# Kernel tuning notes

Hardware: AMD Instinct MI355X
Metric: run time of the kernel (lower is better)

The kernel has to match this reference:

```python
import jax, jax.numpy as jnp
import numpy as np

B, S, D, H = 2, 2048, 1024, 16
DK = D // H


def setup_inputs() -> dict:
    key = jax.random.key(0)
    ks = jax.random.split(key, 11)
    scale = 1.0 / np.sqrt(D)
    inp = {
        "query": jax.random.normal(ks[0], (B, S, D), dtype=jnp.float32),
        "key": jax.random.normal(ks[1], (B, S, D), dtype=jnp.float32),
        "value": jax.random.normal(ks[2], (B, S, D), dtype=jnp.float32),
        "Wq": jax.random.normal(ks[3], (D, D), dtype=jnp.float32) * scale,
        "bq": jnp.zeros((D,), dtype=jnp.float32),
        "Wk": jax.random.normal(ks[4], (D, D), dtype=jnp.float32) * scale,
        "bk": jnp.zeros((D,), dtype=jnp.float32),
        "Wv": jax.random.normal(ks[5], (D, D), dtype=jnp.float32) * scale,
        "bv": jnp.zeros((D,), dtype=jnp.float32),
        "Wo": jax.random.normal(ks[6], (D, D), dtype=jnp.float32) * scale,
        "bo": jnp.zeros((D,), dtype=jnp.float32),
    }
    return inp


def _split_heads(x):
    # [B,S,D] -> [B,H,S,DK]
    b, s, _ = x.shape
    return x.reshape(b, s, H, DK).transpose(0, 2, 1, 3)


def reference(query, key, value, Wq, bq, Wk, bk, Wv, bv, Wo, bo):
    q = _split_heads(query @ Wq.T + bq)
    k = _split_heads(key @ Wk.T + bk)
    v = _split_heads(value @ Wv.T + bv)
    # scaled dot-product attention: [B,H,S,S]
    scores = jnp.einsum("bhqd,bhkd->bhqk", q, k) / np.sqrt(DK).astype(np.float32)
    attn = jax.nn.softmax(scores, axis=-1)  # stable max-subtract softmax, same math
    ctx = jnp.einsum("bhqk,bhkd->bhqd", attn, v)  # [B,H,S,DK]
    ctx = ctx.transpose(0, 2, 1, 3).reshape(query.shape[0], -1, H * DK)
    return ctx @ Wo.T + bo
```

## Files before the change

### kernel.cpp

```cpp
#include <hip/hip_runtime.h>
#include <math.h>

constexpr int NB = 2;
constexpr int NS = 2048;
constexpr int ND = 1024;
constexpr int NH = 16;
constexpr int NDK = 64;

typedef __attribute__((ext_vector_type(8))) short short8;
typedef __attribute__((ext_vector_type(4))) float floatx4;

__device__ inline unsigned short f2bf(float x) {
    unsigned u = __builtin_bit_cast(unsigned, x);
    u += 0x7fffu + ((u >> 16) & 1u);
    return (unsigned short)(u >> 16);
}

__device__ inline uint4 pack8(float4 a, float4 b) {
    unsigned short t[8] = {f2bf(a.x), f2bf(a.y), f2bf(a.z), f2bf(a.w),
                           f2bf(b.x), f2bf(b.y), f2bf(b.z), f2bf(b.w)};
    return *(uint4*)t;
}

#define GLOAD_LDS16(g, l) __builtin_amdgcn_global_load_lds( \
    (const __attribute__((address_space(1))) void*)(g),     \
    (__attribute__((address_space(3))) void*)(l), 16, 0, 0)

#define QSCALE 0.18033688f

__global__ __launch_bounds__(256) void cvt_all(
    const float* __restrict__ s0, const float* __restrict__ s1,
    const float* __restrict__ s2, const float* __restrict__ s3,
    const float* __restrict__ s4, const float* __restrict__ s5,
    const float* __restrict__ s6,
    unsigned short* __restrict__ d0, unsigned short* __restrict__ d1,
    unsigned short* __restrict__ d2, unsigned short* __restrict__ d3,
    unsigned short* __restrict__ d4, unsigned short* __restrict__ d5,
    unsigned short* __restrict__ d6)
{
    const int y = blockIdx.y;
    const float* srcs[7] = {s0, s1, s2, s3, s4, s5, s6};
    unsigned short* dsts[7] = {d0, d1, d2, d3, d4, d5, d6};
    const int nel = (y < 3) ? NB * NS * ND : ND * ND;
    int i = (blockIdx.x * 256 + threadIdx.x) * 8;
    if (i >= nel) return;
    const float* s = srcs[y];
    unsigned short* d = dsts[y];
    float4 a = *(const float4*)(s + i);
    float4 b = *(const float4*)(s + i + 4);
    *(uint4*)(d + i) = pack8(a, b);
}

template<int QA, int QB>
__device__ __forceinline__ void mfma_quad(
    floatx4 (&acc)[8][4], const short8 (&ta)[4][2], const short8 (&tb)[2][2][2])
{
#pragma unroll
    for (int ii = 0; ii < 4; ++ii)
#pragma unroll
        for (int jj = 0; jj < 2; ++jj) {
            acc[QA * 4 + ii][QB * 2 + jj] = __builtin_amdgcn_mfma_f32_16x16x32_bf16(
                ta[ii][0], tb[QB][jj][0], acc[QA * 4 + ii][QB * 2 + jj], 0, 0, 0);
            acc[QA * 4 + ii][QB * 2 + jj] = __builtin_amdgcn_mfma_f32_16x16x32_bf16(
                ta[ii][1], tb[QB][jj][1], acc[QA * 4 + ii][QB * 2 + jj], 0, 0, 0);
        }
}

__global__ __launch_bounds__(512, 2) void gemm_qkv(
    const unsigned short* __restrict__ Xq, const unsigned short* __restrict__ Xk,
    const unsigned short* __restrict__ Xv,
    const unsigned short* __restrict__ Wq, const unsigned short* __restrict__ Wk,
    const unsigned short* __restrict__ Wv,
    const float* __restrict__ bq, const float* __restrict__ bk,
    const float* __restrict__ bv,
    unsigned short* __restrict__ Cq, unsigned short* __restrict__ Ck,
    unsigned short* __restrict__ Cv)
{
    __shared__ unsigned short As[2][256 * 64];
    __shared__ unsigned short Bs[2][256 * 64];

    const int tid = threadIdx.x, w = tid >> 6, lane = tid & 63;
    const int lo = lane & 15, quad = lane >> 4;
    const int bid = blockIdx.x;
    const int seg = bid >> 6;
    const int idx = bid & 63;
    const int xcd = idx & 7;
    const int t8  = idx >> 3;
    const int K = ND;

    int bm, bn;
    const unsigned short *A, *Bw;
    const float* bias;
    if (seg == 2) {
        bm = t8 & 3; bn = (t8 >> 2) * 8 + xcd;
        A = Wv; Bw = Xv; bias = bv;
    } else {
        bn = t8 & 3; bm = (t8 >> 2) * 8 + xcd;
        if (seg == 1) { A = Xk; Bw = Wk; bias = bk; }
        else          { A = Xq; Bw = Wq; bias = bq; }
    }

    const int WM = (w >> 2) * 128, WN = (w & 3) * 64;

    const int srow = tid >> 3;
    const int sgo  = ((tid & 7) ^ (srow & 7)) * 8;
    const unsigned short* Asrc = A  + (size_t)(bm * 256 + srow) * K + sgo;
    const unsigned short* Bsrc = Bw + (size_t)(bn * 256 + srow) * K + sgo;

#define SA(bf_, t_, s_) GLOAD_LDS16(Asrc + (size_t)(s_) * 64 * K + (t_) * 64, \
                                    &As[bf_][(s_) * 4096 + tid * 8])
#define SB(bf_, t_, s_) GLOAD_LDS16(Bsrc + (size_t)(s_) * 64 * K + (t_) * 64, \
                                    &Bs[bf_][(s_) * 4096 + tid * 8])

    const int rp0 = ((quad) ^ (lo & 7)) * 8;
    const int rp1 = ((4 + quad) ^ (lo & 7)) * 8;

    short8 ta[4][2], tb[2][2][2];

#define RDA(bf_, qa_) { _Pragma("unroll") \
    for (int ii = 0; ii < 4; ++ii) { \
        const unsigned short* p_ = &As[bf_][(WM + (qa_) * 64 + ii * 16 + lo) * 64]; \
        ta[ii][0] = *(const short8*)(p_ + rp0); \
        ta[ii][1] = *(const short8*)(p_ + rp1); } }
#define RDB(bf_, qb_) { _Pragma("unroll") \
    for (int jj = 0; jj < 2; ++jj) { \
        const unsigned short* p_ = &Bs[bf_][(WN + (qb_) * 32 + jj * 16 + lo) * 64]; \
        tb[qb_][jj][0] = *(const short8*)(p_ + rp0); \
        tb[qb_][jj][1] = *(const short8*)(p_ + rp1); } }

#define PH_SYNC1 __builtin_amdgcn_s_barrier(); \
    asm volatile("s_waitcnt lgkmcnt(0)" ::: "memory"); \
    __builtin_amdgcn_sched_barrier(0); \
    __builtin_amdgcn_s_setprio(1);
#define PH_SYNC2 __builtin_amdgcn_s_setprio(0); \
    __builtin_amdgcn_sched_barrier(0); \
    __builtin_amdgcn_s_barrier();

    floatx4 acc[8][4];
#pragma unroll
    for (int i = 0; i < 8; ++i)
#pragma unroll
        for (int j = 0; j < 4; ++j) acc[i][j] = (floatx4){0.f, 0.f, 0.f, 0.f};

    SB(0, 0, 0); SB(0, 0, 1); SB(0, 0, 2); SB(0, 0, 3);
    SA(0, 0, 0); SA(0, 0, 1); SA(0, 0, 2); SA(0, 0, 3);
    SB(1, 1, 0); SB(1, 1, 1); SB(1, 1, 2); SB(1, 1, 3);
    asm volatile("s_waitcnt vmcnt(4)" ::: "memory");
    __builtin_amdgcn_s_barrier();

    constexpr int NIT = ND / 128;
#pragma unroll 1
    for (int it = 0; it < NIT; ++it) {
        const bool nl = (it < NIT - 1);
        const int t1 = 2 * it + 1, t2 = 2 * it + 2, t3 = 2 * it + 3;

        RDA(0, 0); RDB(0, 0);
        SA(1, t1, 0); SA(1, t1, 1);
        PH_SYNC1; mfma_quad<0, 0>(acc, ta, tb); PH_SYNC2;

        RDB(0, 1);
        SA(1, t1, 2); SA(1, t1, 3);
        PH_SYNC1; mfma_quad<0, 1>(acc, ta, tb); PH_SYNC2;

        RDA(0, 1);
        if (nl) { SB(0, t2, 0); SB(0, t2, 1); }
        PH_SYNC1; mfma_quad<1, 1>(acc, ta, tb); PH_SYNC2;

        if (nl) { SB(0, t2, 2); SB(0, t2, 3); }
        if (nl) asm volatile("s_waitcnt vmcnt(4)" ::: "memory");
        else    asm volatile("s_waitcnt vmcnt(0)" ::: "memory");
        PH_SYNC1; mfma_quad<1, 0>(acc, ta, tb); PH_SYNC2;

        RDA(1, 0); RDB(1, 0);
        if (nl) { SA(0, t2, 0); SA(0, t2, 1); }
        PH_SYNC1; mfma_quad<0, 0>(acc, ta, tb); PH_SYNC2;

        RDB(1, 1);
        if (nl) { SA(0, t2, 2); SA(0, t2, 3); }
        PH_SYNC1; mfma_quad<0, 1>(acc, ta, tb); PH_SYNC2;

        RDA(1, 1);
        if (nl) { SB(1, t3, 0); SB(1, t3, 1); }
        PH_SYNC1; mfma_quad<1, 1>(acc, ta, tb); PH_SYNC2;

        if (nl) { SB(1, t3, 2); SB(1, t3, 3); }
        if (nl) asm volatile("s_waitcnt vmcnt(4)" ::: "memory");
        PH_SYNC1; mfma_quad<1, 0>(acc, ta, tb); PH_SYNC2;
    }

#undef SA
#undef SB
#undef RDA
#undef RDB
#undef PH_SYNC1
#undef PH_SYNC2

    if (seg < 2) {
        unsigned short* C = seg ? Ck : Cq;
        const float scale = seg ? 1.f : QSCALE;
#pragma unroll
        for (int j = 0; j < 4; ++j) {
            const int col = bn * 256 + WN + j * 16 + lo;
            const float bb = bias[col];
#pragma unroll
            for (int i = 0; i < 8; ++i)
#pragma unroll
                for (int r = 0; r < 4; ++r) {
                    const int row = bm * 256 + WM + i * 16 + quad * 4 + r;
                    C[(size_t)row * ND + col] = f2bf((acc[i][j][r] + bb) * scale);
                }
        }
    } else {
#pragma unroll
        for (int i = 0; i < 8; ++i)
#pragma unroll
            for (int r = 0; r < 4; ++r) {
                const int row = bm * 256 + WM + i * 16 + quad * 4 + r;
                const float bb = bias[row];
#pragma unroll
                for (int j = 0; j < 4; ++j) {
                    const int col = bn * 256 + WN + j * 16 + lo;
                    const int b = col >> 11, s = col & (NS - 1);
                    Cv[(size_t)(b * ND + row) * NS + s] = f2bf(acc[i][j][r] + bb);
                }
            }
    }
}

constexpr int PRS = 72;

__global__ __launch_bounds__(512, 4) void attn_mfma(
    const unsigned short* __restrict__ qb,
    const unsigned short* __restrict__ kb,
    const unsigned short* __restrict__ vt,
    float* __restrict__ cacc0, float* __restrict__ cacc1,
    float* __restrict__ lbuf)
{
    __shared__ unsigned short Ks[2][64 * 64];
    __shared__ unsigned short Vs[2][64 * 64];
    __shared__ unsigned short Pt[8][32 * PRS];

    const int tid = threadIdx.x, w = tid >> 6, lane = tid & 63;
    const int lo = lane & 15, quad = lane >> 4;
    const int bid = blockIdx.x;
    const int xcd = bid & 7;
    const int tt  = bid >> 3;
    const int qgrp = tt & 7;
    const int bhk  = (tt >> 3) * 8 + xcd;
    const int bh = bhk >> 1, ksp = bhk & 1;
    const int b = bh >> 4, h = bh & 15;
    const int q0 = qgrp * 256 + w * 32;

    short8 qf[2][2];
    #pragma unroll
    for (int qt = 0; qt < 2; ++qt) {
        const unsigned short* qrow =
            qb + (size_t)(b * NS + q0 + qt * 16 + lo) * ND + h * NDK + quad * 8;
        qf[qt][0] = *(const short8*)(qrow);
        qf[qt][1] = *(const short8*)(qrow + 32);
    }

    const int r0 = tid >> 3, g0 = (tid & 7) ^ (r0 & 7);
    const unsigned short* Ksrc = kb + (size_t)(b * NS + r0) * ND + h * NDK + g0 * 8;
    const unsigned short* Vsrc = vt + (size_t)(bh * NDK + r0) * NS + g0 * 8;

#define STAGE(bf_, k_) { \
    GLOAD_LDS16(Ksrc + (size_t)(k_) * ND, &Ks[bf_][tid * 8]); \
    GLOAD_LDS16(Vsrc + (k_),              &Vs[bf_][tid * 8]); }

    floatx4 acc[2][4], lacc[2];
    #pragma unroll
    for (int qt = 0; qt < 2; ++qt) {
        lacc[qt] = (floatx4){0.f, 0.f, 0.f, 0.f};
        #pragma unroll
        for (int cb = 0; cb < 4; ++cb) acc[qt][cb] = (floatx4){0.f, 0.f, 0.f, 0.f};
    }

    const short8 ones = {0x3F80, 0x3F80, 0x3F80, 0x3F80,
                         0x3F80, 0x3F80, 0x3F80, 0x3F80};
    unsigned short* pw = &Pt[w][0];
    const int pos0 = (quad ^ (lo & 7)) * 8;
    const int pos1 = ((4 + quad) ^ (lo & 7)) * 8;

    const int kbase = ksp * 1024;
    STAGE(0, kbase);

    #pragma unroll 2
    for (int it = 0; it < 16; ++it) {
        const int bf = it & 1;
        if (it < 15) {
            STAGE(bf ^ 1, kbase + (it + 1) * 64);
            asm volatile("s_waitcnt vmcnt(2)" ::: "memory");
        } else {
            asm volatile("s_waitcnt vmcnt(0)" ::: "memory");
        }
        __builtin_amdgcn_s_barrier();
        __builtin_amdgcn_sched_barrier(0);

        const unsigned short* Kc = Ks[bf];
        const unsigned short* Vc = Vs[bf];

        floatx4 s[2][4];
        __builtin_amdgcn_s_setprio(1);
        #pragma unroll
        for (int t = 0; t < 4; ++t) {
            const int rw = (t * 16 + lo) * 64;
            const short8 kf0 = *(const short8*)(Kc + rw + pos0);
            const short8 kf1 = *(const short8*)(Kc + rw + pos1);
            #pragma unroll
            for (int qt = 0; qt < 2; ++qt) {
                s[qt][t] = __builtin_amdgcn_mfma_f32_16x16x32_bf16(
                    kf0, qf[qt][0], (floatx4){0.f, 0.f, 0.f, 0.f}, 0, 0, 0);
                s[qt][t] = __builtin_amdgcn_mfma_f32_16x16x32_bf16(
                    kf1, qf[qt][1], s[qt][t], 0, 0, 0);
            }
        }
        __builtin_amdgcn_s_setprio(0);

        #pragma unroll
        for (int qt = 0; qt < 2; ++qt)
            #pragma unroll
            for (int t = 0; t < 4; ++t) {
                unsigned u0 = __builtin_bit_cast(unsigned, __builtin_amdgcn_exp2f(s[qt][t][0]));
                unsigned u1 = __builtin_bit_cast(unsigned, __builtin_amdgcn_exp2f(s[qt][t][1]));
                unsigned u2 = __builtin_bit_cast(unsigned, __builtin_amdgcn_exp2f(s[qt][t][2]));
                unsigned u3 = __builtin_bit_cast(unsigned, __builtin_amdgcn_exp2f(s[qt][t][3]));
                uint2 pk = {(u0 >> 16) | (u1 & 0xFFFF0000u),
                            (u2 >> 16) | (u3 & 0xFFFF0000u)};
                *(uint2*)(pw + (qt * 16 + lo) * PRS + t * 16 + quad * 4) = pk;
            }

        short8 pf[2][2];
        #pragma unroll
        for (int qt = 0; qt < 2; ++qt) {
            pf[qt][0] = *(const short8*)(pw + (qt * 16 + lo) * PRS + quad * 8);
            pf[qt][1] = *(const short8*)(pw + (qt * 16 + lo) * PRS + 32 + quad * 8);
            lacc[qt] = __builtin_amdgcn_mfma_f32_16x16x32_bf16(pf[qt][0], ones, lacc[qt], 0, 0, 0);
            lacc[qt] = __builtin_amdgcn_mfma_f32_16x16x32_bf16(pf[qt][1], ones, lacc[qt], 0, 0, 0);
        }

        __builtin_amdgcn_s_setprio(1);
        #pragma unroll
        for (int cb = 0; cb < 4; ++cb) {
            const int rw = (cb * 16 + lo) * 64;
            const short8 vf0 = *(const short8*)(Vc + rw + pos0);
            const short8 vf1 = *(const short8*)(Vc + rw + pos1);
            #pragma unroll
            for (int qt = 0; qt < 2; ++qt) {
                acc[qt][cb] = __builtin_amdgcn_mfma_f32_16x16x32_bf16(pf[qt][0], vf0, acc[qt][cb], 0, 0, 0);
                acc[qt][cb] = __builtin_amdgcn_mfma_f32_16x16x32_bf16(pf[qt][1], vf1, acc[qt][cb], 0, 0, 0);
            }
        }
        __builtin_amdgcn_s_setprio(0);

        __builtin_amdgcn_sched_barrier(0);
        __builtin_amdgcn_s_barrier();
    }
#undef STAGE

    float* ca = ksp ? cacc1 : cacc0;
    float* lb = lbuf + (size_t)ksp * (NB * NH * NS);
    #pragma unroll
    for (int qt = 0; qt < 2; ++qt) {
        #pragma unroll
        for (int cb = 0; cb < 4; ++cb)
            #pragma unroll
            for (int r = 0; r < 4; ++r) {
                size_t off = (size_t)(b * NS + q0 + qt * 16 + quad * 4 + r) * ND
                           + h * NDK + cb * 16 + lo;
                ca[off] = acc[qt][cb][r];
            }
        if (lo == 0)
            #pragma unroll
            for (int r = 0; r < 4; ++r)
                lb[(size_t)bh * NS + q0 + qt * 16 + quad * 4 + r] = lacc[qt][r];
    }
}

__global__ __launch_bounds__(256) void gemm_o(
    const float* __restrict__ cacc0, const float* __restrict__ cacc1,
    const float* __restrict__ lbuf, const unsigned short* __restrict__ Bw,
    const float* __restrict__ bias, float* __restrict__ Cout)
{
    __shared__ unsigned short As[64 * 64];
    __shared__ unsigned short Bs[128 * 64];
    const int tid = threadIdx.x, w = tid >> 6, lane = tid & 63;
    const int lo = lane & 15, quad = lane >> 4;
    const int bid = blockIdx.x;
    const int xcd = bid & 7;
    const int tt  = bid >> 3;
    const int bn  = tt & 7;
    const int bm  = (tt >> 3) * 8 + xcd;
    const int K = ND;
    const int wm = (w >> 1) * 32, wn = (w & 1) * 64;
    const size_t LHALF = (size_t)NB * NH * NS;

    const int ar = tid >> 3;
    const int ag = (tid & 7) ^ (ar & 7);
    const int tok0 = bm * 64 + ar, tok1 = tok0 + 32;
    const float* A00 = cacc0 + (size_t)tok0 * ND + ag * 8;
    const float* A01 = cacc1 + (size_t)tok0 * ND + ag * 8;
    const float* A10 = cacc0 + (size_t)tok1 * ND + ag * 8;
    const float* A11 = cacc1 + (size_t)tok1 * ND + ag * 8;
    const size_t lb0 = (size_t)((tok0 >> 11) << 4) * NS + (tok0 & (NS - 1));
    const size_t lb1 = (size_t)((tok1 >> 11) << 4) * NS + (tok1 & (NS - 1));
    unsigned short* AsD0 = As + tid * 8;
    unsigned short* AsD1 = As + (tid + 256) * 8;

    const unsigned short* Bg[4];
    unsigned short* BsD[4];
    #pragma unroll
    for (int p = 0; p < 4; ++p) {
        int c = tid + 256 * p, r = c >> 3, g = (c & 7) ^ (r & 7);
        Bg[p] = Bw + (size_t)(bn * 128 + r) * K + g * 8;
        BsD[p] = Bs + c * 8;
    }

    floatx4 acc[2][4];
    #pragma unroll
    for (int i = 0; i < 2; ++i)
        #pragma unroll
        for (int j = 0; j < 4; ++j) acc[i][j] = (floatx4){0.f, 0.f, 0.f, 0.f};

    float4 ra[8];
    float lv0, lv1;
    ra[0] = *(const float4*)(A00);     ra[1] = *(const float4*)(A00 + 4);
    ra[2] = *(const float4*)(A01);     ra[3] = *(const float4*)(A01 + 4);
    ra[4] = *(const float4*)(A10);     ra[5] = *(const float4*)(A10 + 4);
    ra[6] = *(const float4*)(A11);     ra[7] = *(const float4*)(A11 + 4);
    lv0 = lbuf[lb0] + lbuf[lb0 + LHALF];
    lv1 = lbuf[lb1] + lbuf[lb1 + LHALF];

    for (int k0 = 0; k0 < K; k0 += 64) {
        const float inv0 = __builtin_amdgcn_rcpf(lv0);
        const float inv1 = __builtin_amdgcn_rcpf(lv1);
        __syncthreads();
        #pragma unroll
        for (int p = 0; p < 4; ++p) GLOAD_LDS16(Bg[p] + k0, BsD[p]);
        {
            float4 s0 = {(ra[0].x + ra[2].x) * inv0, (ra[0].y + ra[2].y) * inv0,
                         (ra[0].z + ra[2].z) * inv0, (ra[0].w + ra[2].w) * inv0};
            float4 s1 = {(ra[1].x + ra[3].x) * inv0, (ra[1].y + ra[3].y) * inv0,
                         (ra[1].z + ra[3].z) * inv0, (ra[1].w + ra[3].w) * inv0};
            *(uint4*)AsD0 = pack8(s0, s1);
            float4 s2 = {(ra[4].x + ra[6].x) * inv1, (ra[4].y + ra[6].y) * inv1,
                         (ra[4].z + ra[6].z) * inv1, (ra[4].w + ra[6].w) * inv1};
            float4 s3 = {(ra[5].x + ra[7].x) * inv1, (ra[5].y + ra[7].y) * inv1,
                         (ra[5].z + ra[7].z) * inv1, (ra[5].w + ra[7].w) * inv1};
            *(uint4*)AsD1 = pack8(s2, s3);
        }
        __syncthreads();

        const int kn = k0 + 64;
        if (kn < K) {
            ra[0] = *(const float4*)(A00 + kn); ra[1] = *(const float4*)(A00 + kn + 4);
            ra[2] = *(const float4*)(A01 + kn); ra[3] = *(const float4*)(A01 + kn + 4);
            ra[4] = *(const float4*)(A10 + kn); ra[5] = *(const float4*)(A10 + kn + 4);
            ra[6] = *(const float4*)(A11 + kn); ra[7] = *(const float4*)(A11 + kn + 4);
            const size_t hoff = (size_t)(kn >> 6) * NS;
            lv0 = lbuf[lb0 + hoff] + lbuf[lb0 + hoff + LHALF];
            lv1 = lbuf[lb1 + hoff] + lbuf[lb1 + hoff + LHALF];
        }

        #pragma unroll
        for (int s = 0; s < 2; ++s) {
            const int pos = ((s * 4 + quad) ^ (lo & 7)) * 8;
            short8 af[2], bf[4];
            #pragma unroll
            for (int i = 0; i < 2; ++i)
                af[i] = *(const short8*)(As + (wm + i * 16 + lo) * 64 + pos);
            #pragma unroll
            for (int j = 0; j < 4; ++j)
                bf[j] = *(const short8*)(Bs + (wn + j * 16 + lo) * 64 + pos);
            #pragma unroll
            for (int i = 0; i < 2; ++i)
                #pragma unroll
                for (int j = 0; j < 4; ++j)
                    acc[i][j] = __builtin_amdgcn_mfma_f32_16x16x32_bf16(af[i], bf[j], acc[i][j], 0, 0, 0);
        }
    }

    #pragma unroll
    for (int j = 0; j < 4; ++j) {
        const int col = bn * 128 + wn + j * 16 + lo;
        const float bb = bias[col];
        #pragma unroll
        for (int i = 0; i < 2; ++i)
            #pragma unroll
            for (int r = 0; r < 4; ++r) {
                const int row = bm * 64 + wm + i * 16 + quad * 4 + r;
                Cout[(size_t)row * ND + col] = acc[i][j][r] + bb;
            }
    }
}

extern "C" void kernel_launch(void* const* d_in, const int* in_sizes, int n_in,
                              void* d_out, int out_size, void* d_ws, size_t ws_size,
                              hipStream_t stream)
{
    const float* query = (const float*)d_in[0];
    const float* key   = (const float*)d_in[1];
    const float* value = (const float*)d_in[2];
    const float* Wq    = (const float*)d_in[3];
    const float* bq    = (const float*)d_in[4];
    const float* Wk    = (const float*)d_in[5];
    const float* bk    = (const float*)d_in[6];
    const float* Wv    = (const float*)d_in[7];
    const float* bv    = (const float*)d_in[8];
    const float* Wo    = (const float*)d_in[9];
    const float* bo    = (const float*)d_in[10];
    float* out = (float*)d_out;

    const size_t n  = (size_t)NB * NS * ND;
    const size_t nw = (size_t)ND * ND;

    unsigned short* X0   = (unsigned short*)d_ws;
    unsigned short* X1   = X0 + n;
    unsigned short* X2   = X1 + n;
    unsigned short* W0   = X2 + n;
    unsigned short* W1   = W0 + nw;
    unsigned short* W2   = W1 + nw;
    unsigned short* W3   = W2 + nw;
    unsigned short* qbuf = W3 + nw;
    unsigned short* kbuf = qbuf + n;
    unsigned short* vtb  = kbuf + n;
    float* cacc1 = (float*)(vtb + n);
    float* lbuf  = cacc1 + n;
    float* cacc0 = (float*)X1;

    cvt_all<<<dim3((int)(n / 2048), 7), 256, 0, stream>>>(
        query, key, value, Wq, Wk, Wv, Wo, X0, X1, X2, W0, W1, W2, W3);

    gemm_qkv<<<192, 512, 0, stream>>>(X0, X1, X2, W0, W1, W2,
                                      bq, bk, bv, qbuf, kbuf, vtb);

    attn_mfma<<<512, 512, 0, stream>>>(qbuf, kbuf, vtb, cacc0, cacc1, lbuf);

    gemm_o<<<512, 256, 0, stream>>>(cacc0, cacc1, lbuf, W3, bo, out);
}
```

Before: 220.0 us.

## Software-pipeline PV matmul one iteration behind exp to overlap MFMA with transcendental

Restructures the attention inner loop so that the P·V MFMAs (and the row-sum MFMAs) for the previous key block run interleaved with the exp2 computation of the current block. V gets a third LDS buffer, rotated by pointer each iteration, and the last block's PV is drained after the loop. The aim is to hide the serial exp/pack latency behind matrix-core work. The cost is extra LDS, live P fragments carried across iterations and more register pressure, which could hurt occupancy at 4 blocks per CU.

```diff
diff --git a/kernel.cpp b/kernel.cpp
--- a/kernel.cpp
+++ b/kernel.cpp
@@ -237,7 +237,7 @@
     float* __restrict__ lbuf)
 {
     __shared__ unsigned short Ks[2][64 * 64];
-    __shared__ unsigned short Vs[2][64 * 64];
+    __shared__ unsigned short Vs[3][64 * 64];
     __shared__ unsigned short Pt[8][32 * PRS];
 
     const int tid = threadIdx.x, w = tid >> 6, lane = tid & 63;
@@ -264,10 +264,6 @@
     const unsigned short* Ksrc = kb + (size_t)(b * NS + r0) * ND + h * NDK + g0 * 8;
     const unsigned short* Vsrc = vt + (size_t)(bh * NDK + r0) * NS + g0 * 8;
 
-#define STAGE(bf_, k_) { \
-    GLOAD_LDS16(Ksrc + (size_t)(k_) * ND, &Ks[bf_][tid * 8]); \
-    GLOAD_LDS16(Vsrc + (k_),              &Vs[bf_][tid * 8]); }
-
     floatx4 acc[2][4], lacc[2];
     #pragma unroll
     for (int qt = 0; qt < 2; ++qt) {
@@ -283,13 +279,20 @@
     const int pos1 = ((4 + quad) ^ (lo & 7)) * 8;
 
     const int kbase = ksp * 1024;
-    STAGE(0, kbase);
+    GLOAD_LDS16(Ksrc + (size_t)kbase * ND, &Ks[0][tid * 8]);
+    GLOAD_LDS16(Vsrc + kbase,              &Vs[0][tid * 8]);
+
+    unsigned short *vp = &Vs[2][0], *vc = &Vs[0][0], *vn = &Vs[1][0];
+
+    short8 pf[2][2];
 
     #pragma unroll 2
     for (int it = 0; it < 16; ++it) {
-        const int bf = it & 1;
+        const int kbuf = it & 1;
         if (it < 15) {
-            STAGE(bf ^ 1, kbase + (it + 1) * 64);
+            const int kk = kbase + (it + 1) * 64;
+            GLOAD_LDS16(Ksrc + (size_t)kk * ND, &Ks[kbuf ^ 1][tid * 8]);
+            GLOAD_LDS16(Vsrc + kk, &vn[tid * 8]);
             asm volatile("s_waitcnt vmcnt(2)" ::: "memory");
         } else {
             asm volatile("s_waitcnt vmcnt(0)" ::: "memory");
@@ -297,8 +300,7 @@
         __builtin_amdgcn_s_barrier();
         __builtin_amdgcn_sched_barrier(0);
 
-        const unsigned short* Kc = Ks[bf];
-        const unsigned short* Vc = Vs[bf];
+        const unsigned short* Kc = Ks[kbuf];
 
         floatx4 s[2][4];
         __builtin_amdgcn_s_setprio(1);
@@ -318,45 +320,62 @@
         __builtin_amdgcn_s_setprio(0);
 
         #pragma unroll
-        for (int qt = 0; qt < 2; ++qt)
-            #pragma unroll
-            for (int t = 0; t < 4; ++t) {
-                unsigned u0 = __builtin_bit_cast(unsigned, __builtin_amdgcn_exp2f(s[qt][t][0]));
-                unsigned u1 = __builtin_bit_cast(unsigned, __builtin_amdgcn_exp2f(s[qt][t][1]));
-                unsigned u2 = __builtin_bit_cast(unsigned, __builtin_amdgcn_exp2f(s[qt][t][2]));
-                unsigned u3 = __builtin_bit_cast(unsigned, __builtin_amdgcn_exp2f(s[qt][t][3]));
+        for (int cb = 0; cb < 4; ++cb) {
+            if (it > 0) {
+                const int rw = (cb * 16 + lo) * 64;
+                const short8 vf0 = *(const short8*)(vp + rw + pos0);
+                const short8 vf1 = *(const short8*)(vp + rw + pos1);
+                __builtin_amdgcn_s_setprio(1);
+                #pragma unroll
+                for (int qt = 0; qt < 2; ++qt) {
+                    acc[qt][cb] = __builtin_amdgcn_mfma_f32_16x16x32_bf16(
+                        pf[qt][0], vf0, acc[qt][cb], 0, 0, 0);
+                    acc[qt][cb] = __builtin_amdgcn_mfma_f32_16x16x32_bf16(
+                        pf[qt][1], vf1, acc[qt][cb], 0, 0, 0);
+                }
+                lacc[cb >> 1] = __builtin_amdgcn_mfma_f32_16x16x32_bf16(
+                    pf[cb >> 1][cb & 1], ones, lacc[cb >> 1], 0, 0, 0);
+                __builtin_amdgcn_s_setprio(0);
+            }
+            #pragma unroll
+            for (int qt = 0; qt < 2; ++qt) {
+                unsigned u0 = __builtin_bit_cast(unsigned, __builtin_amdgcn_exp2f(s[qt][cb][0]));
+                unsigned u1 = __builtin_bit_cast(unsigned, __builtin_amdgcn_exp2f(s[qt][cb][1]));
+                unsigned u2 = __builtin_bit_cast(unsigned, __builtin_amdgcn_exp2f(s[qt][cb][2]));
+                unsigned u3 = __builtin_bit_cast(unsigned, __builtin_amdgcn_exp2f(s[qt][cb][3]));
                 uint2 pk = {(u0 >> 16) | (u1 & 0xFFFF0000u),
                             (u2 >> 16) | (u3 & 0xFFFF0000u)};
-                *(uint2*)(pw + (qt * 16 + lo) * PRS + t * 16 + quad * 4) = pk;
+                *(uint2*)(pw + (qt * 16 + lo) * PRS + cb * 16 + quad * 4) = pk;
             }
-
-        short8 pf[2][2];
+        }
+
         #pragma unroll
         for (int qt = 0; qt < 2; ++qt) {
             pf[qt][0] = *(const short8*)(pw + (qt * 16 + lo) * PRS + quad * 8);
             pf[qt][1] = *(const short8*)(pw + (qt * 16 + lo) * PRS + 32 + quad * 8);
-            lacc[qt] = __builtin_amdgcn_mfma_f32_16x16x32_bf16(pf[qt][0], ones, lacc[qt], 0, 0, 0);
-            lacc[qt] = __builtin_amdgcn_mfma_f32_16x16x32_bf16(pf[qt][1], ones, lacc[qt], 0, 0, 0);
-        }
-
-        __builtin_amdgcn_s_setprio(1);
-        #pragma unroll
-        for (int cb = 0; cb < 4; ++cb) {
-            const int rw = (cb * 16 + lo) * 64;
-            const short8 vf0 = *(const short8*)(Vc + rw + pos0);
-            const short8 vf1 = *(const short8*)(Vc + rw + pos1);
-            #pragma unroll
-            for (int qt = 0; qt < 2; ++qt) {
-                acc[qt][cb] = __builtin_amdgcn_mfma_f32_16x16x32_bf16(pf[qt][0], vf0, acc[qt][cb], 0, 0, 0);
-                acc[qt][cb] = __builtin_amdgcn_mfma_f32_16x16x32_bf16(pf[qt][1], vf1, acc[qt][cb], 0, 0, 0);
-            }
-        }
-        __builtin_amdgcn_s_setprio(0);
+        }
 
         __builtin_amdgcn_sched_barrier(0);
         __builtin_amdgcn_s_barrier();
-    }
-#undef STAGE
+
+        unsigned short* t_ = vp; vp = vc; vc = vn; vn = t_;
+    }
+
+    #pragma unroll
+    for (int cb = 0; cb < 4; ++cb) {
+        const int rw = (cb * 16 + lo) * 64;
+        const short8 vf0 = *(const short8*)(vp + rw + pos0);
+        const short8 vf1 = *(const short8*)(vp + rw + pos1);
+        #pragma unroll
+        for (int qt = 0; qt < 2; ++qt) {
+            acc[qt][cb] = __builtin_amdgcn_mfma_f32_16x16x32_bf16(
+                pf[qt][0], vf0, acc[qt][cb], 0, 0, 0);
+            acc[qt][cb] = __builtin_amdgcn_mfma_f32_16x16x32_bf16(
+                pf[qt][1], vf1, acc[qt][cb], 0, 0, 0);
+        }
+        lacc[cb >> 1] = __builtin_amdgcn_mfma_f32_16x16x32_bf16(
+            pf[cb >> 1][cb & 1], ones, lacc[cb >> 1], 0, 0, 0);
+    }
 
     float* ca = ksp ? cacc1 : cacc0;
     float* lb = lbuf + (size_t)ksp * (NB * NH * NS);
```

Measured after the change: 232.0 us. +5.5%, slower.

## Load K and V fragments directly from global memory, dropping LDS staging

Applied to the files above, without the earlier changes.

Removes the double-buffered LDS staging of K and V tiles (async global-to-LDS loads, waitcnt and block barriers) and has each wave read its MFMA K/V fragments straight from global memory. The row-sum MFMAs are also moved into the PV loop so they interleave with it. This drops the barriers and the LDS traffic, but each of the 8 waves now fetches the same K/V data separately, relying on cache, and there is no prefetch to hide load latency.

```diff
diff --git a/kernel.cpp b/kernel.cpp
--- a/kernel.cpp
+++ b/kernel.cpp
@@ -236,8 +236,6 @@
     float* __restrict__ cacc0, float* __restrict__ cacc1,
     float* __restrict__ lbuf)
 {
-    __shared__ unsigned short Ks[2][64 * 64];
-    __shared__ unsigned short Vs[2][64 * 64];
     __shared__ unsigned short Pt[8][32 * PRS];
 
     const int tid = threadIdx.x, w = tid >> 6, lane = tid & 63;
@@ -260,14 +258,6 @@
         qf[qt][1] = *(const short8*)(qrow + 32);
     }
 
-    const int r0 = tid >> 3, g0 = (tid & 7) ^ (r0 & 7);
-    const unsigned short* Ksrc = kb + (size_t)(b * NS + r0) * ND + h * NDK + g0 * 8;
-    const unsigned short* Vsrc = vt + (size_t)(bh * NDK + r0) * NS + g0 * 8;
-
-#define STAGE(bf_, k_) { \
-    GLOAD_LDS16(Ksrc + (size_t)(k_) * ND, &Ks[bf_][tid * 8]); \
-    GLOAD_LDS16(Vsrc + (k_),              &Vs[bf_][tid * 8]); }
-
     floatx4 acc[2][4], lacc[2];
     #pragma unroll
     for (int qt = 0; qt < 2; ++qt) {
@@ -279,34 +269,24 @@
     const short8 ones = {0x3F80, 0x3F80, 0x3F80, 0x3F80,
                          0x3F80, 0x3F80, 0x3F80, 0x3F80};
     unsigned short* pw = &Pt[w][0];
-    const int pos0 = (quad ^ (lo & 7)) * 8;
-    const int pos1 = ((4 + quad) ^ (lo & 7)) * 8;
 
     const int kbase = ksp * 1024;
-    STAGE(0, kbase);
+    const unsigned short* kp = kb + (size_t)(b * NS + kbase + lo) * ND
+                                  + h * NDK + quad * 8;
+    const unsigned short* vp = vt + (size_t)(bh * NDK + lo) * NS
+                                  + kbase + quad * 8;
 
     #pragma unroll 2
     for (int it = 0; it < 16; ++it) {
-        const int bf = it & 1;
-        if (it < 15) {
-            STAGE(bf ^ 1, kbase + (it + 1) * 64);
-            asm volatile("s_waitcnt vmcnt(2)" ::: "memory");
-        } else {
-            asm volatile("s_waitcnt vmcnt(0)" ::: "memory");
-        }
-        __builtin_amdgcn_s_barrier();
-        __builtin_amdgcn_sched_barrier(0);
-
-        const unsigned short* Kc = Ks[bf];
-        const unsigned short* Vc = Vs[bf];
+        const int ko = it * 64;
 
         floatx4 s[2][4];
         __builtin_amdgcn_s_setprio(1);
         #pragma unroll
         for (int t = 0; t < 4; ++t) {
-            const int rw = (t * 16 + lo) * 64;
-            const short8 kf0 = *(const short8*)(Kc + rw + pos0);
-            const short8 kf1 = *(const short8*)(Kc + rw + pos1);
+            const unsigned short* ka = kp + (size_t)(ko + t * 16) * ND;
+            const short8 kf0 = *(const short8*)(ka);
+            const short8 kf1 = *(const short8*)(ka + 32);
             #pragma unroll
             for (int qt = 0; qt < 2; ++qt) {
                 s[qt][t] = __builtin_amdgcn_mfma_f32_16x16x32_bf16(
@@ -335,28 +315,26 @@
         for (int qt = 0; qt < 2; ++qt) {
             pf[qt][0] = *(const short8*)(pw + (qt * 16 + lo) * PRS + quad * 8);
             pf[qt][1] = *(const short8*)(pw + (qt * 16 + lo) * PRS + 32 + quad * 8);
-            lacc[qt] = __builtin_amdgcn_mfma_f32_16x16x32_bf16(pf[qt][0], ones, lacc[qt], 0, 0, 0);
-            lacc[qt] = __builtin_amdgcn_mfma_f32_16x16x32_bf16(pf[qt][1], ones, lacc[qt], 0, 0, 0);
         }
 
         __builtin_amdgcn_s_setprio(1);
         #pragma unroll
         for (int cb = 0; cb < 4; ++cb) {
-            const int rw = (cb * 16 + lo) * 64;
-            const short8 vf0 = *(const short8*)(Vc + rw + pos0);
-            const short8 vf1 = *(const short8*)(Vc + rw + pos1);
+            const unsigned short* va = vp + (size_t)(cb * 16) * NS + ko;
+            const short8 vf0 = *(const short8*)(va);
+            const short8 vf1 = *(const short8*)(va + 32);
             #pragma unroll
             for (int qt = 0; qt < 2; ++qt) {
-                acc[qt][cb] = __builtin_amdgcn_mfma_f32_16x16x32_bf16(pf[qt][0], vf0, acc[qt][cb], 0, 0, 0);
-                acc[qt][cb] = __builtin_amdgcn_mfma_f32_16x16x32_bf16(pf[qt][1], vf1, acc[qt][cb], 0, 0, 0);
+                acc[qt][cb] = __builtin_amdgcn_mfma_f32_16x16x32_bf16(
+                    pf[qt][0], vf0, acc[qt][cb], 0, 0, 0);
+                acc[qt][cb] = __builtin_amdgcn_mfma_f32_16x16x32_bf16(
+                    pf[qt][1], vf1, acc[qt][cb], 0, 0, 0);
             }
+            lacc[cb >> 1] = __builtin_amdgcn_mfma_f32_16x16x32_bf16(
+                pf[cb >> 1][cb & 1], ones, lacc[cb >> 1], 0, 0, 0);
         }
         __builtin_amdgcn_s_setprio(0);
-
-        __builtin_amdgcn_sched_barrier(0);
-        __builtin_amdgcn_s_barrier();
-    }
-#undef STAGE
+    }
 
     float* ca = ksp ? cacc1 : cacc0;
     float* lb = lbuf + (size_t)ksp * (NB * NH * NS);
```

Result: slower. 298.4 us (+35.7%).

## Double-buffer weight tiles in output projection GEMM with async prefetch

Applied to the files above, without the earlier changes.

The output projection GEMM now keeps two LDS buffers for the weight tile and issues the next tile's global-to-LDS loads before working on the current one. Explicit vmcnt/lgkmcnt waits and raw barriers replace the two __syncthreads per step. s_setprio is raised around the MFMA section. This aims to hide weight-load latency behind compute, at the cost of extra LDS, a third barrier per iteration and hand-tuned wait counts that depend on load ordering.

```diff
diff --git a/kernel.cpp b/kernel.cpp
--- a/kernel.cpp
+++ b/kernel.cpp
@@ -383,7 +383,7 @@
     const float* __restrict__ bias, float* __restrict__ Cout)
 {
     __shared__ unsigned short As[64 * 64];
-    __shared__ unsigned short Bs[128 * 64];
+    __shared__ unsigned short Bs[2][128 * 64];
     const int tid = threadIdx.x, w = tid >> 6, lane = tid & 63;
     const int lo = lane & 15, quad = lane >> 4;
     const int bid = blockIdx.x;
@@ -408,12 +408,12 @@
     unsigned short* AsD1 = As + (tid + 256) * 8;
 
     const unsigned short* Bg[4];
-    unsigned short* BsD[4];
+    int bsoff[4];
     #pragma unroll
     for (int p = 0; p < 4; ++p) {
         int c = tid + 256 * p, r = c >> 3, g = (c & 7) ^ (r & 7);
         Bg[p] = Bw + (size_t)(bn * 128 + r) * K + g * 8;
-        BsD[p] = Bs + c * 8;
+        bsoff[p] = c * 8;
     }
 
     floatx4 acc[2][4];
@@ -421,6 +421,9 @@
     for (int i = 0; i < 2; ++i)
         #pragma unroll
         for (int j = 0; j < 4; ++j) acc[i][j] = (floatx4){0.f, 0.f, 0.f, 0.f};
+
+    #pragma unroll
+    for (int p = 0; p < 4; ++p) GLOAD_LDS16(Bg[p], &Bs[0][bsoff[p]]);
 
     float4 ra[8];
     float lv0, lv1;
@@ -431,12 +434,22 @@
     lv0 = lbuf[lb0] + lbuf[lb0 + LHALF];
     lv1 = lbuf[lb1] + lbuf[lb1 + LHALF];
 
-    for (int k0 = 0; k0 < K; k0 += 64) {
+    #pragma unroll 1
+    for (int t = 0; t < 16; ++t) {
+        const int k0 = t * 64;
+        const int cur = t & 1;
+        if (t < 15) {
+            #pragma unroll
+            for (int p = 0; p < 4; ++p)
+                GLOAD_LDS16(Bg[p] + k0 + 64, &Bs[cur ^ 1][bsoff[p]]);
+        }
         const float inv0 = __builtin_amdgcn_rcpf(lv0);
         const float inv1 = __builtin_amdgcn_rcpf(lv1);
-        __syncthreads();
-        #pragma unroll
-        for (int p = 0; p < 4; ++p) GLOAD_LDS16(Bg[p] + k0, BsD[p]);
+        if (t < 15) asm volatile("s_waitcnt vmcnt(4)" ::: "memory");
+        else        asm volatile("s_waitcnt vmcnt(0)" ::: "memory");
+        __builtin_amdgcn_s_barrier();
+        __builtin_amdgcn_sched_barrier(0);
+
         {
             float4 s0 = {(ra[0].x + ra[2].x) * inv0, (ra[0].y + ra[2].y) * inv0,
                          (ra[0].z + ra[2].z) * inv0, (ra[0].w + ra[2].w) * inv0};
@@ -449,10 +462,9 @@
                          (ra[5].z + ra[7].z) * inv1, (ra[5].w + ra[7].w) * inv1};
             *(uint4*)AsD1 = pack8(s2, s3);
         }
-        __syncthreads();
-
-        const int kn = k0 + 64;
-        if (kn < K) {
+
+        if (t < 15) {
+            const int kn = k0 + 64;
             ra[0] = *(const float4*)(A00 + kn); ra[1] = *(const float4*)(A00 + kn + 4);
             ra[2] = *(const float4*)(A01 + kn); ra[3] = *(const float4*)(A01 + kn + 4);
             ra[4] = *(const float4*)(A10 + kn); ra[5] = *(const float4*)(A10 + kn + 4);
@@ -462,6 +474,11 @@
             lv1 = lbuf[lb1 + hoff] + lbuf[lb1 + hoff + LHALF];
         }
 
+        asm volatile("s_waitcnt lgkmcnt(0)" ::: "memory");
+        __builtin_amdgcn_sched_barrier(0);
+        __builtin_amdgcn_s_barrier();
+
+        __builtin_amdgcn_s_setprio(1);
         #pragma unroll
         for (int s = 0; s < 2; ++s) {
             const int pos = ((s * 4 + quad) ^ (lo & 7)) * 8;
@@ -471,13 +488,16 @@
                 af[i] = *(const short8*)(As + (wm + i * 16 + lo) * 64 + pos);
             #pragma unroll
             for (int j = 0; j < 4; ++j)
-                bf[j] = *(const short8*)(Bs + (wn + j * 16 + lo) * 64 + pos);
+                bf[j] = *(const short8*)(&Bs[cur][(wn + j * 16 + lo) * 64] + pos);
             #pragma unroll
             for (int i = 0; i < 2; ++i)
                 #pragma unroll
                 for (int j = 0; j < 4; ++j)
                     acc[i][j] = __builtin_amdgcn_mfma_f32_16x16x32_bf16(af[i], bf[j], acc[i][j], 0, 0, 0);
         }
+        __builtin_amdgcn_s_setprio(0);
+        __builtin_amdgcn_sched_barrier(0);
+        __builtin_amdgcn_s_barrier();
     }
 
     #pragma unroll
```

Result: no change. 219.2 us (-0.4%).
